# Kernel optimization log

Hardware: AMD Instinct MI355X
Metric: run time of the kernel (lower is better)

Reference implementation:

```python
import jax, jax.numpy as jnp
import numpy as np

BS, Q, NC, T = 32, 600, 152, 32


def cxcywh_to_xyxy(b):
    cx, cy, w, h = b[..., 0], b[..., 1], b[..., 2], b[..., 3]
    return jnp.stack([cx - 0.5 * w, cy - 0.5 * h, cx + 0.5 * w, cy + 0.5 * h], axis=-1)


def generalized_box_iou(b1, b2):
    # b1: [N,4], b2: [M,4] in xyxy. Returns [N,M] GIoU.
    area1 = (b1[:, 2] - b1[:, 0]) * (b1[:, 3] - b1[:, 1])
    area2 = (b2[:, 2] - b2[:, 0]) * (b2[:, 3] - b2[:, 1])
    lt = jnp.maximum(b1[:, None, :2], b2[None, :, :2])
    rb = jnp.minimum(b1[:, None, 2:], b2[None, :, 2:])
    wh = jnp.clip(rb - lt, 0.0)
    inter = wh[..., 0] * wh[..., 1]
    union = area1[:, None] + area2[None, :] - inter
    iou = inter / union
    ltc = jnp.minimum(b1[:, None, :2], b2[None, :, :2])
    rbc = jnp.maximum(b1[:, None, 2:], b2[None, :, 2:])
    whc = jnp.clip(rbc - ltc, 0.0)
    areac = whc[..., 0] * whc[..., 1]
    return iou - (areac - union) / areac


def build_cost(logits, boxes, tgt_ids, tgt_bbox, wc=1.0, wb=1.0, wg=1.0):
    # logits [bs,Q,NC], boxes [bs,Q,4] cxcywh; tgt_ids [bs*T], tgt_bbox [bs*T,4].
    bs, q, _ = logits.shape
    prob = jax.nn.softmax(logits.reshape(bs * q, -1), axis=-1)
    cost_class = -prob[:, tgt_ids]                                  # [bs*Q, bs*T]
    ob = boxes.reshape(bs * q, 4)
    cost_bbox = jnp.abs(ob[:, None, :] - tgt_bbox[None, :, :]).sum(-1)  # L1 cdist
    cost_giou = -generalized_box_iou(cxcywh_to_xyxy(ob), cxcywh_to_xyxy(tgt_bbox))
    C = wb * cost_bbox + wc * cost_class + wg * cost_giou
    return C.reshape(bs, q, -1)


def lsa(cost):
    # Exact rectangular linear sum assignment (Jonker-Volgenant shortest
    # augmenting path with potentials). cost: np [n, m], n <= m.
    # Returns (rows, cols): matched pairs sorted by col index.
    n, m = cost.shape
    INF = 1e18
    u = np.zeros(n + 1)
    v = np.zeros(m + 1)
    p = np.zeros(m + 1, dtype=np.int64)   # p[j] = row matched to col j (1-based)
    way = np.zeros(m + 1, dtype=np.int64)
    for i in range(1, n + 1):
        p[0] = i
        j0 = 0
        minv = np.full(m + 1, INF)
        used = np.zeros(m + 1, dtype=bool)
        while True:
            used[j0] = True
            i0 = p[j0]
            free = np.where(~used)[0]
            cur = cost[i0 - 1, free - 1] - u[i0] - v[free]
            better = cur < minv[free]
            minv[free] = np.where(better, cur, minv[free])
            way[free] = np.where(better, j0, way[free])
            k = int(np.argmin(minv[free]))
            delta = minv[free][k]
            j1 = int(free[k])
            uidx = np.where(used)[0]
            u[p[uidx]] += delta
            v[uidx] -= delta
            minv[free] -= delta
            j0 = j1
            if p[j0] == 0:
                break
        while j0 != 0:
            j1 = int(way[j0])
            p[j0] = p[j1]
            j0 = j1
    cols = np.where(p[1:] != 0)[0]
    rows = p[1:][cols] - 1
    return rows, cols


def match(C_np):
    # C_np: [bs, Q, bs*T]; use diagonal target blocks like torch split-by-sizes.
    pred_idx, tgt_idx = [], []
    for b in range(BS):
        block = C_np[b, :, b * T:(b + 1) * T].T      # [T, Q], T <= Q
        r, c = lsa(block)                            # r: target idx, c: pred idx
        pred_idx.append(c)
        tgt_idx.append(r)
    return jnp.asarray(np.stack(pred_idx)), jnp.asarray(np.stack(tgt_idx))


def setup_inputs() -> dict:
    key = jax.random.key(0)
    ks = jax.random.split(key, 8)
    return {
        "pred_sub_logits": jax.random.normal(ks[0], (BS, Q, NC), jnp.float32),
        "pred_obj_logits": jax.random.normal(ks[1], (BS, Q, NC), jnp.float32),
        "pred_boxes_sub": jax.random.uniform(ks[2], (BS, Q, 4), jnp.float32),
        "pred_boxes_obj": jax.random.uniform(ks[3], (BS, Q, 4), jnp.float32),
        "tgt_sub_bbox": jax.random.uniform(ks[4], (BS, T, 4), jnp.float32),
        "tgt_obj_bbox": jax.random.uniform(ks[5], (BS, T, 4), jnp.float32),
        "tgt_sub_ids": jax.random.randint(ks[6], (BS, T), 0, NC, jnp.int64),
        "tgt_obj_ids": jax.random.randint(ks[7], (BS, T), 0, NC, jnp.int64),
    }


def reference(pred_sub_logits, pred_obj_logits, pred_boxes_sub, pred_boxes_obj,
              tgt_sub_bbox, tgt_obj_bbox, tgt_sub_ids, tgt_obj_ids):
    ids_s = tgt_sub_ids.reshape(-1)
    ids_o = tgt_obj_ids.reshape(-1)
    C_sub = build_cost(pred_sub_logits, pred_boxes_sub, ids_s, tgt_sub_bbox.reshape(-1, 4))
    C_obj = build_cost(pred_obj_logits, pred_boxes_obj, ids_o, tgt_obj_bbox.reshape(-1, 4))
    # Host-side exact Hungarian per batch element (mirrors scipy
    # linear_sum_assignment on the CPU-transferred cost matrix).
    Cs_np = np.asarray(C_sub, dtype=np.float64)
    Co_np = np.asarray(C_obj, dtype=np.float64)
    ps, ts = match(Cs_np)
    po, to = match(Co_np)
    return (C_sub, C_obj, ps, ts, po, to)
```

## Files before the change

kernel.cpp:

```cpp
#include <hip/hip_runtime.h>
#include <math.h>

#define BS 32
#define Q  600
#define NC 152
#define T  32
#define MT (BS*T)
#define CM_SIZE ((size_t)BS*Q*MT)
#define NSLOT 10
#define FBIG 1e30f

typedef float vfloat4 __attribute__((ext_vector_type(4)));

__global__ __launch_bounds__(256) void cost_kernel(
    const float* __restrict__ logits_s, const float* __restrict__ logits_o,
    const float* __restrict__ boxes_s,  const float* __restrict__ boxes_o,
    const float* __restrict__ tbb_s,    const float* __restrict__ tbb_o,
    const int*   __restrict__ tids_s,   const int*   __restrict__ tids_o,
    float* __restrict__ C_s, float* __restrict__ C_o,
    float* __restrict__ blockT, int use_staged)
{
    const int w = threadIdx.x >> 6, lane = threadIdx.x & 63;
    const int rowg = blockIdx.x * 4 + w;
    const int mat = rowg / (BS * Q);
    const int r   = rowg % (BS * Q);
    const int b = r / Q, q = r % Q;

    const float* logits = mat ? logits_o : logits_s;
    const float* boxes  = mat ? boxes_o  : boxes_s;
    const float* tbb    = mat ? tbb_o    : tbb_s;
    const int*   tids   = mat ? tids_o   : tids_s;
    float* C = mat ? C_o : C_s;

    const float* lrow = logits + (size_t)r * NC;
    const float l0 = (lane       < NC) ? lrow[lane]       : -INFINITY;
    const float l1 = (lane + 64  < NC) ? lrow[lane + 64]  : -INFINITY;
    const float l2 = (lane + 128 < NC) ? lrow[lane + 128] : -INFINITY;
    float m = fmaxf(l0, fmaxf(l1, l2));
    #pragma unroll
    for (int off = 32; off > 0; off >>= 1) m = fmaxf(m, __shfl_xor(m, off));
    const float e0 = __expf(l0 - m), e1 = __expf(l1 - m), e2 = __expf(l2 - m);
    float s = e0 + e1 + e2;
    #pragma unroll
    for (int off = 32; off > 0; off >>= 1) s += __shfl_xor(s, off);
    const float inv = 1.0f / s;

    __shared__ float sprob[4][NC];
    if (lane       < NC) sprob[w][lane]       = e0 * inv;
    if (lane + 64  < NC) sprob[w][lane + 64]  = e1 * inv;
    if (lane + 128 < NC) sprob[w][lane + 128] = e2 * inv;
    __syncthreads();

    const float4 ob = ((const float4*)boxes)[r];
    const float ocx = ob.x, ocy = ob.y, ow = ob.z, oh = ob.w;
    const float ox1 = ocx - 0.5f*ow, oy1 = ocy - 0.5f*oh;
    const float ox2 = ocx + 0.5f*ow, oy2 = ocy + 0.5f*oh;
    const float area1 = ow * oh;

    float* Crow = C + (size_t)r * MT;
    float* bT   = blockT + ((size_t)mat*BS + b) * T * Q;

    #pragma unroll
    for (int it = 0; it < 4; ++it) {
        const int t0 = it*256 + lane*4;
        const int4 cls4 = ((const int4*)tids)[t0 >> 2];
        const bool stg = use_staged && ((t0 >> 5) == b);
        vfloat4 res;
        #pragma unroll
        for (int k = 0; k < 4; ++k) {
            const int t = t0 + k;
            const int cls = (&cls4.x)[k];
            const float cc = -sprob[w][cls];

            const float4 tb = ((const float4*)tbb)[t];
            const float cb = fabsf(ocx-tb.x) + fabsf(ocy-tb.y)
                           + fabsf(ow -tb.z) + fabsf(oh -tb.w);

            const float tx1 = fmaf(-0.5f, tb.z, tb.x), ty1 = fmaf(-0.5f, tb.w, tb.y);
            const float tx2 = fmaf( 0.5f, tb.z, tb.x), ty2 = fmaf( 0.5f, tb.w, tb.y);
            const float area2 = tb.z * tb.w;

            const float ltx = fmaxf(ox1,tx1), lty = fmaxf(oy1,ty1);
            const float rbx = fminf(ox2,tx2), rby = fminf(oy2,ty2);
            const float iw = fmaxf(rbx-ltx, 0.0f), ih = fmaxf(rby-lty, 0.0f);
            const float inter = iw*ih;
            const float uni = area1 + area2 - inter;

            const float cx1 = fminf(ox1,tx1), cy1 = fminf(oy1,ty1);
            const float cx2 = fmaxf(ox2,tx2), cy2 = fmaxf(oy2,ty2);
            const float areac = (cx2-cx1)*(cy2-cy1);

            const float giou = inter * __builtin_amdgcn_rcpf(uni)
                             - (areac - uni) * __builtin_amdgcn_rcpf(areac);

            const float cost = cb + cc - giou;
            res[k] = cost;
            if (stg) bT[(size_t)(t & 31)*Q + q] = cost;
        }
        __builtin_nontemporal_store(res, (vfloat4*)(Crow + t0));
    }
}

__device__ __forceinline__ unsigned wave_min_u32(unsigned x) {
  int v = (int)x;
  #define ST(CTRL, RMASK) { \
    int p = __builtin_amdgcn_update_dpp(v, v, CTRL, RMASK, 0xF, false); \
    v = ((unsigned)p < (unsigned)v) ? p : v; }
  ST(0xB1, 0xF)
  ST(0x4E, 0xF)
  ST(0x141, 0xF)
  ST(0x140, 0xF)
  ST(0x142, 0xA)
  ST(0x143, 0xC)
  #undef ST
  return (unsigned)__builtin_amdgcn_readlane(v, 63);
}

__device__ __forceinline__ unsigned f32_sortable(float f) {
  unsigned u = __float_as_uint(f);
  return u ^ ((unsigned)((int)u >> 31) | 0x80000000u);
}
__device__ __forceinline__ float f32_unsortable(unsigned s) {
  unsigned m = (unsigned)((int)(~s) >> 31) | 0x80000000u;
  return __uint_as_float(s ^ m);
}

__global__ __launch_bounds__(64) void lsa_kernel(
    const float* __restrict__ blockT, const float* __restrict__ Cbase,
    float* __restrict__ idx_out, int use_staged)
{
    const int prob = blockIdx.x;
    const int mat = prob >> 5, b = prob & 31;
    const int lane = threadIdx.x;

    __shared__ float clds[T * Q];
    __shared__ float u_s[T + 1];

    if (use_staged) {
        const float4* src = (const float4*)(blockT + (size_t)prob * T * Q);
        float4* dst = (float4*)clds;
        for (int idx = lane; idx < (T*Q)/4; idx += 64)
            dst[idx] = src[idx];
    } else {
        const float* cbk = Cbase + (size_t)mat*CM_SIZE + (size_t)b*Q*MT + (size_t)b*T;
        for (int t = 0; t < T; ++t)
            for (int q = lane; q < Q; q += 64)
                clds[t*Q + q] = cbk[(size_t)q * MT + t];
    }
    if (lane <= T) u_s[lane] = 0.0f;
    __syncthreads();

    float vreg[NSLOT], minv[NSLOT];
    int   wayreg[NSLOT], low[NSLOT];
    int   pcol[NSLOT];
    #pragma unroll
    for (int c = 0; c < NSLOT; ++c) { vreg[c] = 0.0f; pcol[c] = 0; }

    for (int i = 1; i <= T; ++i) {
        #pragma unroll
        for (int c = 0; c < NSLOT; ++c) {
            const int q0 = c*64 + lane;
            minv[c] = FBIG;
            wayreg[c] = 0;
            low[c] = (q0 < Q) ? (((q0 + 1) << 6) | pcol[c]) : 0x3FFFFF;
        }
        unsigned usedmask = 0;
        float Dcum = 0.0f;
        int j0 = 0, i0 = i, jfin;

        while (true) {
            const float u0 = u_s[i0];
            const float* crow = clds + (i0 - 1) * Q;

            float cst[NSLOT];
            #pragma unroll
            for (int c = 0; c < NSLOT; ++c) {
                const int q0 = c*64 + lane;
                cst[c] = (q0 < Q) ? crow[q0] : FBIG;
            }
            const float sh = Dcum - u0;

            float bm[NSLOT];
            #pragma unroll
            for (int c = 0; c < NSLOT; ++c) {
                const bool fre = !((usedmask >> c) & 1u);
                const float cur = (cst[c] - vreg[c]) + sh;
                const bool upd = fre && (cur < minv[c]);
                wayreg[c] = upd ? j0 : wayreg[c];
                minv[c]   = upd ? cur : minv[c];
                bm[c] = fre ? minv[c] : FBIG;
            }
            const float m0 = fminf(bm[0], fminf(bm[1], bm[2]));
            const float m1 = fminf(bm[3], fminf(bm[4], bm[5]));
            const float m2 = fminf(bm[6], fminf(bm[7], bm[8]));
            const float best = fminf(fminf(m0, m1), fminf(m2, bm[9]));
            int blow = 0x3FFFFF;
            #pragma unroll
            for (int c = NSLOT - 1; c >= 0; --c) blow = (bm[c] == best) ? low[c] : blow;

            const unsigned sb = f32_sortable(best);
            const unsigned gb = wave_min_u32(sb);
            const unsigned long long mask = __ballot(sb == gb);
            int blow_w;
            if (__popcll(mask) == 1) {
                blow_w = __builtin_amdgcn_readlane(blow, __ffsll(mask) - 1);
            } else {
                const unsigned cand = (sb == gb) ? (unsigned)blow : 0x3FFFFFu;
                blow_w = (int)wave_min_u32(cand);
            }

            Dcum = f32_unsortable(gb);
            const int j1  = (blow_w >> 6) & 0x3FF;
            const int pj1 = blow_w & 0x3F;

            if (pj1 == 0) { jfin = j1; break; }
            const int owner1 = (j1 - 1) & 63, slot1 = (j1 - 1) >> 6;
            if (lane == owner1) usedmask |= 1u << slot1;
            j0 = j1; i0 = pj1;
        }

        const float Dfin = Dcum;
        #pragma unroll
        for (int c = 0; c < NSLOT; ++c) {
            if ((usedmask >> c) & 1u) {
                const float dec = Dfin - minv[c];
                vreg[c] -= dec;
                u_s[low[c] & 63] += dec;
            }
        }
        if (lane == 0) u_s[i] += Dfin;

        int jj = jfin;
        while (jj) {
            const int owner = (jj - 1) & 63, slot = (jj - 1) >> 6;
            int wv = 0;
            #pragma unroll
            for (int c = 0; c < NSLOT; ++c) if (slot == c) wv = wayreg[c];
            const int jw = __shfl(wv, owner);
            int newp;
            if (jw == 0) newp = i;
            else {
                const int ow2 = (jw - 1) & 63, sl2 = (jw - 1) >> 6;
                int pv2 = 0;
                #pragma unroll
                for (int c = 0; c < NSLOT; ++c) if (sl2 == c) pv2 = low[c] & 63;
                newp = __shfl(pv2, ow2);
            }
            if (lane == owner) {
                #pragma unroll
                for (int c = 0; c < NSLOT; ++c) if (slot == c) pcol[c] = newp;
            }
            jj = jw;
        }
    }

    float* pred = idx_out + (size_t)mat * 2 * BS * T;
    float* tgt  = pred + BS * T;
    int base = 0;
    #pragma unroll
    for (int c = 0; c < NSLOT; ++c) {
        const int q0 = c*64 + lane;
        const int pj = (q0 < Q) ? pcol[c] : 0;
        const bool mtch = (q0 < Q) && (pj != 0);
        const unsigned long long mask = __ballot(mtch);
        if (mtch) {
            const int pos = base + __popcll(mask & ((1ull << lane) - 1ull));
            pred[b*T + pos] = (float)q0;
            tgt [b*T + pos] = (float)(pj - 1);
        }
        base += __popcll(mask);
    }
}

extern "C" void kernel_launch(void* const* d_in, const int* in_sizes, int n_in,
                              void* d_out, int out_size, void* d_ws, size_t ws_size,
                              hipStream_t stream) {
    const float* logits_s = (const float*)d_in[0];
    const float* logits_o = (const float*)d_in[1];
    const float* boxes_s  = (const float*)d_in[2];
    const float* boxes_o  = (const float*)d_in[3];
    const float* tbb_s    = (const float*)d_in[4];
    const float* tbb_o    = (const float*)d_in[5];
    const int*   tids_s   = (const int*)d_in[6];
    const int*   tids_o   = (const int*)d_in[7];

    float* out = (float*)d_out;
    float* C_s = out;
    float* C_o = out + CM_SIZE;
    float* idx_out = out + 2*CM_SIZE;

    const size_t staged_bytes = (size_t)2*BS*T*Q*sizeof(float);
    const int use_staged = (ws_size >= staged_bytes) ? 1 : 0;
    float* blockT = (float*)d_ws;

    cost_kernel<<<(2*BS*Q)/4, 256, 0, stream>>>(logits_s, logits_o, boxes_s, boxes_o,
                                                tbb_s, tbb_o, tids_s, tids_o,
                                                C_s, C_o, blockT, use_staged);

    lsa_kernel<<<64, 64, 0, stream>>>(blockT, C_s, idx_out, use_staged);
}
```

Baseline: 290.7 us.

## Add greedy column-reduction initialization before Hungarian augmenting loop

Before the shortest-augmenting-path phase, each row's minimum cost column is found with a wave reduction, the row potential is set to that minimum, and the row is greedily assigned if that column is free. Only the rows that could not be assigned this way run the full Dijkstra-style augmentation. This targets the serial augmentation cost per row, at the price of an extra pass over the cost rows. Correctness depends on the greedy initial potentials and assignments staying consistent with the dual feasibility that JV needs.

```diff
diff --git a/kernel.cpp b/kernel.cpp
--- a/kernel.cpp
+++ b/kernel.cpp
@@ -156,7 +156,48 @@
     #pragma unroll
     for (int c = 0; c < NSLOT; ++c) { vreg[c] = 0.0f; pcol[c] = 0; }
 
+    unsigned um = 0;
     for (int i = 1; i <= T; ++i) {
+        const float* crow = clds + (i - 1) * Q;
+        float bm[NSLOT];
+        #pragma unroll
+        for (int c = 0; c < NSLOT; ++c) {
+            const int q0 = c*64 + lane;
+            bm[c] = (q0 < Q) ? crow[q0] : FBIG;
+        }
+        const float m0 = fminf(bm[0], fminf(bm[1], bm[2]));
+        const float m1 = fminf(bm[3], fminf(bm[4], bm[5]));
+        const float m2 = fminf(bm[6], fminf(bm[7], bm[8]));
+        const float best = fminf(fminf(m0, m1), fminf(m2, bm[9]));
+        const unsigned gb = wave_min_u32(f32_sortable(best));
+        const float gbf = f32_unsortable(gb);
+
+        if (lane == 0) u_s[i] = gbf;
+
+        int cand = 0x7FFFFFFF;
+        #pragma unroll
+        for (int c = NSLOT - 1; c >= 0; --c)
+            cand = (bm[c] == gbf) ? (c*64 + lane) : cand;
+        const int jm = (int)wave_min_u32((unsigned)cand);
+
+        const int owner = jm & 63, slot = jm >> 6;
+        int pv = 0;
+        #pragma unroll
+        for (int c = 0; c < NSLOT; ++c) if (slot == c) pv = pcol[c];
+        const int cur = __shfl(pv, owner);
+        if (cur == 0) {
+            if (lane == owner) {
+                #pragma unroll
+                for (int c = 0; c < NSLOT; ++c) if (slot == c) pcol[c] = i;
+            }
+        } else {
+            um |= 1u << (i - 1);
+        }
+    }
+
+    for (int i = 1; i <= T; ++i) {
+        if (!((um >> (i - 1)) & 1u)) continue;
+
         #pragma unroll
         for (int c = 0; c < NSLOT; ++c) {
             const int q0 = c*64 + lane;
```

Result: faster. 275.1 us (-5.4%).
